# Performance work log

Measured on AMD Instinct MI355X. Metric: run time of the kernel, lower is better.

Reference implementation:

```python
import jax, jax.numpy as jnp
import numpy as np

N = 8192; E = 131072; K = 20; IN_DIM = 3; HID = 256; N_CLASSES = 32


def setup_inputs():
    key = jax.random.key(0)
    ks = jax.random.split(key, 16)

    def w(k, shape):
        lim = 1.0 / np.sqrt(shape[0])
        return jax.random.uniform(k, shape, jnp.float32, -lim, lim)

    f32 = jnp.float32
    return {
        "features": jax.random.normal(ks[0], (N, IN_DIM), f32),
        "src": jax.random.randint(ks[1], (E,), 0, N, jnp.int32),
        "dst": jax.random.randint(ks[2], (E,), 0, N, jnp.int32),
        # GraphConv params
        "Wc1": w(ks[3], (IN_DIM, HID)), "bc1": jnp.zeros((HID,), f32),
        "Wc2": w(ks[4], (HID, HID)), "bc2": jnp.zeros((HID,), f32),
        "Wc3": w(ks[5], (64, N_CLASSES)), "bc3": jnp.zeros((N_CLASSES,), f32),
        # DynamicEdgeConv 1 MLP: [2*256 -> 256 -> 256], Linear+BN+ReLU each
        "W11": w(ks[6], (2 * HID, 256)), "b11": jnp.zeros((256,), f32), "g11": jnp.ones((256,), f32), "be11": jnp.zeros((256,), f32),
        "W12": w(ks[7], (256, 256)), "b12": jnp.zeros((256,), f32), "g12": jnp.ones((256,), f32), "be12": jnp.zeros((256,), f32),
        # DynamicEdgeConv 2 MLP: [2*256 -> 64 -> 64]
        "W21": w(ks[8], (2 * 256, 64)), "b21": jnp.zeros((64,), f32), "g21": jnp.ones((64,), f32), "be21": jnp.zeros((64,), f32),
        "W22": w(ks[9], (64, 64)), "b22": jnp.zeros((64,), f32), "g22": jnp.ones((64,), f32), "be22": jnp.zeros((64,), f32),
    }


def reference(features, src, dst, Wc1, bc1, Wc2, bc2, Wc3, bc3,
              W11, b11, g11, be11, W12, b12, g12, be12,
              W21, b21, g21, be21, W22, b22, g22, be22):
    n = features.shape[0]
    ones_e = jnp.ones(src.shape[0], features.dtype)
    # DGL GraphConv norm='both': deg clamped to min 1
    dout = jnp.clip(jax.ops.segment_sum(ones_e, src, num_segments=n), 1.0) ** -0.5
    din = jnp.clip(jax.ops.segment_sum(ones_e, dst, num_segments=n), 1.0) ** -0.5

    def gconv(x, W, b, act):
        agg = jax.ops.segment_sum((x * dout[:, None])[src], dst, num_segments=n)
        r = (agg * din[:, None]) @ W + b
        return jax.nn.relu(r) if act else r

    def bn(x, g, b):  # BatchNorm1d in training mode over all edge rows
        mu = jnp.mean(x, axis=(0, 1), keepdims=True)
        var = jnp.mean(jnp.square(x - mu), axis=(0, 1), keepdims=True)
        return (x - mu) * jax.lax.rsqrt(var + 1e-5) * g + b

    def edge_conv(x, layers):
        # dynamic kNN graph on current features (self included, dist 0)
        sq = jnp.sum(x * x, axis=-1)
        d = sq[:, None] + sq[None, :] - 2.0 * (x @ x.T)  # [N,N]
        idx = jax.lax.top_k(-d, K)[1]                    # [N,K]
        xi = x[:, None, :]
        e = jnp.concatenate([jnp.broadcast_to(xi, (n, K, x.shape[-1])), x[idx] - xi], axis=-1)  # [N,K,2F]
        for W, b, g, be in layers:
            e = jax.nn.relu(bn(e @ W + b, g, be))
        return jnp.max(e, axis=1)  # max aggregation over neighbors

    h = gconv(features, Wc1, bc1, True)                                   # [N,256]
    h = edge_conv(h, [(W11, b11, g11, be11), (W12, b12, g12, be12)])      # [N,256]
    h = gconv(h, Wc2, bc2, True)                                          # [N,256]
    h = edge_conv(h, [(W21, b21, g21, be21), (W22, b22, g22, be22)])      # [N,64]
    return gconv(h, Wc3, bc3, False)                                      # [N,32]
```

## Files before the change

kernel.cpp:

```cpp
#include <hip/hip_runtime.h>

#define NN 8192
#define NE 131072
#define KNN 20
#define CH 4096
#define GBM 128
#define GBN 128
#define GBK 64

typedef __attribute__((ext_vector_type(4))) float f32x4;
typedef __attribute__((ext_vector_type(8))) __bf16 bf16x8;

__global__ void k_zero(float* p, int n){
  int i = blockIdx.x*256 + threadIdx.x;
  if (i < n) p[i] = 0.f;
}
__global__ void k_zero_i(int* p, int n){
  int i = blockIdx.x*256 + threadIdx.x;
  if (i < n) p[i] = 0;
}

__device__ __forceinline__ unsigned short f2bf(float x){
  unsigned u = __float_as_uint(x);
  unsigned r = (u + 0x7fff + ((u >> 16) & 1)) >> 16;
  return (unsigned short)r;
}
__device__ __forceinline__ float bf2f(unsigned short h){
  return __uint_as_float((unsigned)h << 16);
}
__device__ __forceinline__ void gload16(const void* g, void* l){
  __builtin_amdgcn_global_load_lds(
      (const __attribute__((address_space(1))) void*)g,
      (__attribute__((address_space(3))) void*)l, 16, 0, 0);
}

__global__ void k_count(const int* __restrict__ src, const int* __restrict__ dst,
                        int* cs, int* cd){
  int e = blockIdx.x*256 + threadIdx.x;
  if (e < NE){ atomicAdd(&cs[src[e]], 1); atomicAdd(&cd[dst[e]], 1); }
}
__global__ void k_deg(const int* cs, const int* cd, float* dout, float* din){
  int i = blockIdx.x*256 + threadIdx.x;
  if (i < NN){
    dout[i] = rsqrtf((float)max(cs[i], 1));
    din[i]  = rsqrtf((float)max(cd[i], 1));
  }
}
__global__ void k_scan(const int* __restrict__ cnt, int* __restrict__ off){
  __shared__ int sh[256];
  __shared__ int carry;
  int tid = threadIdx.x;
  if (tid == 0) carry = 0;
  __syncthreads();
  for (int base = 0; base < NN; base += 256){
    int v = cnt[base + tid];
    int x = v;
    sh[tid] = x; __syncthreads();
    for (int o = 1; o < 256; o <<= 1){
      int y = (tid >= o) ? sh[tid - o] : 0;
      __syncthreads();
      x += y; sh[tid] = x;
      __syncthreads();
    }
    off[base + tid] = carry + x - v;
    __syncthreads();
    if (tid == 255){
      carry += x;
      if (base + 256 == NN) off[NN] = carry;
    }
    __syncthreads();
  }
}
__global__ void k_fill(const int* __restrict__ src, const int* __restrict__ dst,
                       const int* __restrict__ roff, int* cursor, int* csr){
  int e = blockIdx.x*256 + threadIdx.x;
  if (e < NE){
    int d = dst[e];
    int p = atomicAdd(&cursor[d], 1);
    csr[roff[d] + p] = src[e];
  }
}

__global__ void k_gconv1(const float* __restrict__ feat, const int* __restrict__ roff,
                         const int* __restrict__ csr, const float* __restrict__ dout,
                         const float* __restrict__ din, const float* __restrict__ Wc1,
                         const float* __restrict__ bc1, float* __restrict__ h1){
  int wid = threadIdx.x >> 6, lane = threadIdx.x & 63;
  int i = blockIdx.x*4 + wid;
  float a0=0.f, a1=0.f, a2=0.f;
  int beg = roff[i], end = roff[i+1];
  for (int t = beg + lane; t < end; t += 64){
    int s = csr[t]; float w = dout[s];
    a0 += feat[s*3+0]*w; a1 += feat[s*3+1]*w; a2 += feat[s*3+2]*w;
  }
  for (int m = 32; m; m >>= 1){
    a0 += __shfl_xor(a0, m); a1 += __shfl_xor(a1, m); a2 += __shfl_xor(a2, m);
  }
  float dn = din[i];
  a0 *= dn; a1 *= dn; a2 *= dn;
  for (int c = lane; c < 256; c += 64){
    float r = a0*Wc1[c] + a1*Wc1[256+c] + a2*Wc1[512+c] + bc1[c];
    h1[(size_t)i*256 + c] = fmaxf(r, 0.f);
  }
}

__global__ void k_sq(const float* __restrict__ X, float* __restrict__ sq){
  int wid = threadIdx.x >> 6, lane = threadIdx.x & 63;
  int i = blockIdx.x*4 + wid;
  float4 v = *(const float4*)&X[(size_t)i*256 + lane*4];
  float s = v.x*v.x + v.y*v.y + v.z*v.z + v.w*v.w;
  for (int m = 32; m; m >>= 1) s += __shfl_xor(s, m);
  if (lane == 0) sq[i] = s;
}

__global__ void k_split(const float* __restrict__ X, unsigned short* __restrict__ xcat){
  int row = blockIdx.x, c = threadIdx.x;
  float x = X[(size_t)row*256 + c];
  unsigned short h = f2bf(x);
  unsigned short lo = f2bf(x - bf2f(h));
  xcat[(size_t)row*512 + c] = h;
  xcat[(size_t)row*512 + 256 + c] = lo;
}

__global__ __launch_bounds__(256)
void k_gram_mfma(const unsigned short* __restrict__ Xcat,
                 float* __restrict__ G, int r0){
  __shared__ unsigned short sA[GBM*GBK];
  __shared__ unsigned short sB[GBM*GBK];
  int tid = threadIdx.x;
  int lw = tid >> 6, l = tid & 63;
  int rbl = blockIdx.y*GBM;
  int rb = r0 + rbl;
  int cb = blockIdx.x*GBN;

  int srow = l >> 3;
  int scol = (l & 7) ^ srow;
  const unsigned short* srcA[4];
  const unsigned short* srcB[4];
  char* dstA[4]; char* dstB[4];
  #pragma unroll
  for (int i = 0; i < 4; i++){
    int c = lw*4 + i;
    int row = c*8 + srow;
    srcA[i] = Xcat + (size_t)(rb + row)*512 + scol*8;
    srcB[i] = Xcat + (size_t)(cb + row)*512 + scol*8;
    dstA[i] = (char*)sA + c*1024;
    dstB[i] = (char*)sB + c*1024;
  }

  int wm = lw >> 1, wn = lw & 1;
  int fm = l & 15, kg = l >> 4;
  unsigned offA[4][2], offB[4][2];
  #pragma unroll
  for (int mf = 0; mf < 4; mf++){
    int rowa = wm*64 + mf*16 + fm;
    int rowb = wn*64 + mf*16 + fm;
    #pragma unroll
    for (int ks = 0; ks < 2; ks++){
      offA[mf][ks] = rowa*128 + (((unsigned)(ks*4 + kg) ^ (rowa & 7)))*16;
      offB[mf][ks] = rowb*128 + (((unsigned)(ks*4 + kg) ^ (rowb & 7)))*16;
    }
  }

  f32x4 acc[4][4];
  #pragma unroll
  for (int m = 0; m < 4; m++)
    #pragma unroll
    for (int n = 0; n < 4; n++) acc[m][n] = (f32x4){0.f,0.f,0.f,0.f};

  #pragma unroll
  for (int s = 0; s < 12; s++){
    int sec = s >> 2;
    int inner = (s & 3)*64;
    int cbA = (sec == 1 ? 256 : 0) + inner;
    int cbB = (sec == 2 ? 256 : 0) + inner;
    #pragma unroll
    for (int i = 0; i < 4; i++){
      gload16(srcA[i] + cbA, dstA[i]);
      gload16(srcB[i] + cbB, dstB[i]);
    }
    __syncthreads();
    #pragma unroll
    for (int ks = 0; ks < 2; ks++){
      bf16x8 a[4], b[4];
      #pragma unroll
      for (int mf = 0; mf < 4; mf++) a[mf] = *(const bf16x8*)((const char*)sA + offA[mf][ks]);
      #pragma unroll
      for (int nf = 0; nf < 4; nf++) b[nf] = *(const bf16x8*)((const char*)sB + offB[nf][ks]);
      #pragma unroll
      for (int mf = 0; mf < 4; mf++)
        #pragma unroll
        for (int nf = 0; nf < 4; nf++)
          acc[mf][nf] = __builtin_amdgcn_mfma_f32_16x16x32_bf16(a[mf], b[nf], acc[mf][nf], 0, 0, 0);
    }
    __syncthreads();
  }

  #pragma unroll
  for (int mf = 0; mf < 4; mf++){
    int orow = rbl + wm*64 + mf*16 + kg*4;
    #pragma unroll
    for (int nf = 0; nf < 4; nf++){
      int ocol = cb + wn*64 + nf*16 + fm;
      #pragma unroll
      for (int r = 0; r < 4; r++)
        G[(size_t)(orow + r)*NN + ocol] = acc[mf][nf][r];
    }
  }
}

__global__ __launch_bounds__(256)
void k_topk(const float* __restrict__ G, const float* __restrict__ sq,
            int r0, int* __restrict__ idxo){
  __shared__ float lsq[NN];
  int tid = threadIdx.x;
  for (int t = tid; t < NN/4; t += 256)
    ((float4*)lsq)[t] = ((const float4*)sq)[t];
  __syncthreads();

  int wid = tid >> 6, lane = tid & 63;
  int rl = blockIdx.x*4 + wid;
  int gr = r0 + rl;
  const float4* row4 = (const float4*)(G + (size_t)rl*NN);
  const float4* lsq4 = (const float4*)lsq;
  float sqr = lsq[gr];

  float kd0=INFINITY,kd1=INFINITY,kd2=INFINITY,kd3=INFINITY,kd4=INFINITY,
        kd5=INFINITY,kd6=INFINITY,kd7=INFINITY,kd8=INFINITY,kd9=INFINITY,
        kd10=INFINITY,kd11=INFINITY,kd12=INFINITY,kd13=INFINITY,kd14=INFINITY,
        kd15=INFINITY,kd16=INFINITY,kd17=INFINITY,kd18=INFINITY,kd19=INFINITY;
  int ki0=0x7fffffff,ki1=0x7fffffff,ki2=0x7fffffff,ki3=0x7fffffff,ki4=0x7fffffff,
      ki5=0x7fffffff,ki6=0x7fffffff,ki7=0x7fffffff,ki8=0x7fffffff,ki9=0x7fffffff,
      ki10=0x7fffffff,ki11=0x7fffffff,ki12=0x7fffffff,ki13=0x7fffffff,ki14=0x7fffffff,
      ki15=0x7fffffff,ki16=0x7fffffff,ki17=0x7fffffff,ki18=0x7fffffff,ki19=0x7fffffff;

#define ST(U) { bool sw = nk < kd##U; float tv = kd##U; int tq = ki##U; \
      if (sw){ kd##U = nk; ki##U = ni; nk = tv; ni = tq; } }
#define INSE(kc, jc) { if ((kc) < kd19){ float nk = (kc); int ni = (jc); \
      ST(0) ST(1) ST(2) ST(3) ST(4) ST(5) ST(6) ST(7) ST(8) ST(9) \
      ST(10) ST(11) ST(12) ST(13) ST(14) ST(15) ST(16) ST(17) ST(18) ST(19) } }

  #pragma unroll 1
  for (int o = 0; o < 32; o++){
    int t4 = lane + o*64;
    float4 g = row4[t4];
    float4 s = lsq4[t4];
    int jb = t4*4;
    float k0 = (sqr + s.x) - 2.f*g.x;
    float k1 = (sqr + s.y) - 2.f*g.y;
    float k2 = (sqr + s.z) - 2.f*g.z;
    float k3 = (sqr + s.w) - 2.f*g.w;
    float t19 = kd19;
    float mn = fminf(fminf(k0,k1), fminf(k2,k3));
    if (__any(mn < t19)){
      INSE(k0, jb+0);
      INSE(k1, jb+1);
      INSE(k2, jb+2);
      INSE(k3, jb+3);
    }
  }
#undef INSE
#undef ST

#define MV(A,B) { kd##A = kd##B; ki##A = ki##B; }
  #pragma unroll 1
  for (int r = 0; r < KNN; r++){
    float bv = kd0; int bi = ki0;
    #pragma unroll
    for (int mm = 32; mm; mm >>= 1){
      float ov = __shfl_xor(bv, mm); int oi = __shfl_xor(bi, mm);
      if (ov < bv || (ov == bv && oi < bi)){ bv = ov; bi = oi; }
    }
    if (ki0 == bi){
      MV(0,1) MV(1,2) MV(2,3) MV(3,4) MV(4,5) MV(5,6) MV(6,7) MV(7,8) MV(8,9) MV(9,10)
      MV(10,11) MV(11,12) MV(12,13) MV(13,14) MV(14,15) MV(15,16) MV(16,17) MV(17,18) MV(18,19)
      kd19 = INFINITY; ki19 = 0x7fffffff;
    }
    if (lane == 0) idxo[(size_t)gr*KNN + r] = bi;
  }
#undef MV
}

__global__ void k_wd(const float* __restrict__ W, float* __restrict__ Wd, int rows, int M){
  int t = blockIdx.x*256 + threadIdx.x;
  if (t < rows*M) Wd[t] = W[t] - W[rows*M + t];
}

__global__ __launch_bounds__(256)
void k_mm(const float* __restrict__ A, const float* __restrict__ B,
          const float* __restrict__ bias, float* __restrict__ Cout,
          int n, int Kd, int M, int relu){
  __shared__ float la[16][68], lb[16][68];
  int tid = threadIdx.x;
  int rb = blockIdx.y*64, cb = blockIdx.x*64;
  int lr = tid >> 2, lq = (tid & 3)*4;
  int ty = tid >> 4, tx = tid & 15;
  float acc[4][4] = {};
  for (int k0 = 0; k0 < Kd; k0 += 16){
    __syncthreads();
    #pragma unroll
    for (int u = 0; u < 4; u++){
      int k = k0 + lq + u;
      la[lq+u][lr] = (k < Kd) ? A[(size_t)(rb+lr)*Kd + k] : 0.f;
    }
    int kk = tid >> 4; int cc = (tid & 15)*4;
    #pragma unroll
    for (int u = 0; u < 4; u++){
      int c = cb + cc + u; int k = k0 + kk;
      lb[kk][cc+u] = (k < Kd && c < M) ? B[(size_t)k*M + c] : 0.f;
    }
    __syncthreads();
    #pragma unroll
    for (int k = 0; k < 16; k++){
      float4 a = *(const float4*)&la[k][ty*4];
      float4 b = *(const float4*)&lb[k][tx*4];
      float avv[4] = {a.x,a.y,a.z,a.w}, bvv[4] = {b.x,b.y,b.z,b.w};
      #pragma unroll
      for (int u = 0; u < 4; u++)
        #pragma unroll
        for (int v = 0; v < 4; v++) acc[u][v] += avv[u]*bvv[v];
    }
  }
  #pragma unroll
  for (int u = 0; u < 4; u++){
    int r = rb + ty*4 + u;
    #pragma unroll
    for (int v = 0; v < 4; v++){
      int c = cb + tx*4 + v;
      if (c < M){
        float x = acc[u][v] + (bias ? bias[c] : 0.f);
        if (relu) x = fmaxf(x, 0.f);
        Cout[(size_t)r*M + c] = x;
      }
    }
  }
}

template<int C>
__global__ __launch_bounds__(256)
void k_stats1(const float* __restrict__ A, const float* __restrict__ P,
              const int* __restrict__ idx, float* __restrict__ ssum, float* __restrict__ ssq){
  __shared__ int si[128], sj[128];
  int tid = threadIdx.x;
  int s0 = blockIdx.x*128;
  if (tid < 128){ si[tid] = (s0 + tid)/KNN; sj[tid] = idx[s0 + tid]; }
  __syncthreads();
  constexpr int MPAR = 256/C;
  int tc = tid % C, sr = tid / C;
  float s = 0.f, q = 0.f;
  for (int m = sr; m < 128; m += MPAR){
    float v = A[(size_t)si[m]*C + tc] + P[(size_t)sj[m]*C + tc];
    s += v; q += v*v;
  }
  if constexpr (MPAR > 1){
    __shared__ float rs[256], rq[256];
    rs[tid] = s; rq[tid] = q; __syncthreads();
    if (sr == 0){
      for (int u = 1; u < MPAR; u++){ s += rs[u*C + tc]; q += rq[u*C + tc]; }
    }
  }
  if (sr == 0){ atomicAdd(&ssum[tc], s); atomicAdd(&ssq[tc], q); }
}

template<int C>
__global__ __launch_bounds__(256)
void k_colstats(const float* __restrict__ X, float* __restrict__ ssum, float* __restrict__ ssq){
  constexpr int MPAR = 256/C;
  int tid = threadIdx.x;
  int tc = tid % C, sr = tid / C;
  int base = blockIdx.x*256;
  float s = 0.f, q = 0.f;
  for (int m = sr; m < 256; m += MPAR){
    float v = X[(size_t)(base + m)*C + tc];
    s += v; q += v*v;
  }
  if constexpr (MPAR > 1){
    __shared__ float rs[256], rq[256];
    rs[tid] = s; rq[tid] = q; __syncthreads();
    if (sr == 0){
      for (int u = 1; u < MPAR; u++){ s += rs[u*C + tc]; q += rq[u*C + tc]; }
    }
  }
  if (sr == 0){ atomicAdd(&ssum[tc], s); atomicAdd(&ssq[tc], q); }
}

__global__ void k_bn_final(const float* __restrict__ ssum, const float* __restrict__ ssq,
                           const float* __restrict__ g, const float* __restrict__ be,
                           float* __restrict__ sb, float* __restrict__ tb, int C, float invn){
  int c = threadIdx.x;
  if (c < C){
    float mu = ssum[c]*invn;
    float var = fmaxf(ssq[c]*invn - mu*mu, 0.f);
    float s = g[c]*rsqrtf(var + 1e-5f);
    sb[c] = s; tb[c] = be[c] - mu*s;
  }
}

template<int C>
__global__ __launch_bounds__(256)
void k_edge_mm(const float* __restrict__ A, const float* __restrict__ P,
               const int* __restrict__ idx, const float* __restrict__ sb,
               const float* __restrict__ tb, const float* __restrict__ W,
               const float* __restrict__ bias, float* __restrict__ out){
  constexpr int BM   = (C == 256) ? 32 : 64;
  constexpr int KT   = (C == 256) ? 16 : 64;
  constexpr int COLG = C/8;
  constexpr int ROWG = 256/COLG;
  constexpr int EPT  = BM/ROWG;
  constexpr int MPAR = 256/C;
  __shared__ float e2[BM][C+1];
  __shared__ float wt[KT][C+4];
  __shared__ int sj[BM];
  int tid = threadIdx.x;
  int s0 = blockIdx.x*BM;
  if (tid < BM) sj[tid] = idx[s0 + tid];
  __syncthreads();
  for (int mb = 0; mb < BM; mb += MPAR){
    int m = mb + tid / C;
    int c = tid % C;
    int i = (s0 + m)/KNN;
    int j = sj[m];
    float v = (A[(size_t)i*C + c] + P[(size_t)j*C + c])*sb[c] + tb[c];
    e2[m][c] = fmaxf(v, 0.f);
  }
  float acc[EPT][8];
  #pragma unroll
  for (int m = 0; m < EPT; m++)
    #pragma unroll
    for (int u = 0; u < 8; u++) acc[m][u] = 0.f;
  int tr = tid / COLG, tc = tid % COLG;
  for (int kt = 0; kt < C; kt += KT){
    __syncthreads();
    for (int t = tid; t < KT*C; t += 256){
      wt[t / C][t % C] = W[(size_t)(kt + t/C)*C + (t % C)];
    }
    __syncthreads();
    #pragma unroll 4
    for (int k = 0; k < KT; k++){
      float4 w0 = *(const float4*)&wt[k][tc*8];
      float4 w1 = *(const float4*)&wt[k][tc*8 + 4];
      float b[8] = {w0.x,w0.y,w0.z,w0.w,w1.x,w1.y,w1.z,w1.w};
      #pragma unroll
      for (int m = 0; m < EPT; m++){
        float a = e2[tr*EPT + m][kt + k];
        #pragma unroll
        for (int u = 0; u < 8; u++) acc[m][u] += a*b[u];
      }
    }
  }
  #pragma unroll
  for (int m = 0; m < EPT; m++){
    int row = s0 + tr*EPT + m;
    float4 o0, o1;
    o0.x = acc[m][0] + bias[tc*8+0]; o0.y = acc[m][1] + bias[tc*8+1];
    o0.z = acc[m][2] + bias[tc*8+2]; o0.w = acc[m][3] + bias[tc*8+3];
    o1.x = acc[m][4] + bias[tc*8+4]; o1.y = acc[m][5] + bias[tc*8+5];
    o1.z = acc[m][6] + bias[tc*8+6]; o1.w = acc[m][7] + bias[tc*8+7];
    *(float4*)&out[(size_t)row*C + tc*8]     = o0;
    *(float4*)&out[(size_t)row*C + tc*8 + 4] = o1;
  }
}

template<int C>
__global__ void k_maxpool(const float* __restrict__ X, const float* __restrict__ sb,
                          const float* __restrict__ tb, float* __restrict__ H){
  constexpr int NPB = 256/C;
  int node = blockIdx.x*NPB + threadIdx.x / C;
  int c = threadIdx.x % C;
  float s = sb[c], t = tb[c];
  float mx = 0.f;
  for (int k = 0; k < KNN; k++){
    float v = X[(size_t)(node*KNN + k)*C + c]*s + t;
    mx = fmaxf(mx, v);
  }
  H[(size_t)node*C + c] = mx;
}

template<int C>
__global__ void k_agg(const float* __restrict__ X, const int* __restrict__ roff,
                      const int* __restrict__ csr, const float* __restrict__ dout,
                      const float* __restrict__ din, float* __restrict__ XA){
  int i = blockIdx.x; int c = threadIdx.x;
  float acc = 0.f;
  int b = roff[i], e = roff[i+1];
  for (int t = b; t < e; t++){
    int s = csr[t];
    acc += X[(size_t)s*C + c]*dout[s];
  }
  XA[(size_t)i*C + c] = acc*din[i];
}

extern "C" void kernel_launch(void* const* d_in, const int* in_sizes, int n_in,
                              void* d_out, int out_size, void* d_ws, size_t ws_size,
                              hipStream_t stream){
  const float* feat = (const float*)d_in[0];
  const int*   src  = (const int*)d_in[1];
  const int*   dst  = (const int*)d_in[2];
  const float* Wc1  = (const float*)d_in[3];
  const float* bc1  = (const float*)d_in[4];
  const float* Wc2  = (const float*)d_in[5];
  const float* bc2  = (const float*)d_in[6];
  const float* Wc3  = (const float*)d_in[7];
  const float* bc3  = (const float*)d_in[8];
  const float* W11  = (const float*)d_in[9];
  const float* b11  = (const float*)d_in[10];
  const float* g11  = (const float*)d_in[11];
  const float* be11 = (const float*)d_in[12];
  const float* W12  = (const float*)d_in[13];
  const float* b12  = (const float*)d_in[14];
  const float* g12  = (const float*)d_in[15];
  const float* be12 = (const float*)d_in[16];
  const float* W21  = (const float*)d_in[17];
  const float* b21  = (const float*)d_in[18];
  const float* g21  = (const float*)d_in[19];
  const float* be21 = (const float*)d_in[20];
  const float* W22  = (const float*)d_in[21];
  const float* b22  = (const float*)d_in[22];
  const float* g22  = (const float*)d_in[23];
  const float* be22 = (const float*)d_in[24];
  float* out = (float*)d_out;

  char* w = (char*)d_ws; size_t off = 0;
  auto alloc = [&](size_t bytes)->void*{
    void* p = w + off;
    off += bytes; off = (off + 255) & ~(size_t)255;
    return p;
  };
  int* cnt_s  = (int*)alloc(NN*4);
  int* cnt_d  = (int*)alloc(NN*4);
  int* roff   = (int*)alloc((NN+1)*4);
  int* cursor = (int*)alloc(NN*4);
  int* csr    = (int*)alloc(NE*4);
  int* idx    = (int*)alloc((size_t)NN*KNN*4);
  float* dout = (float*)alloc(NN*4);
  float* din  = (float*)alloc(NN*4);
  float* sqv  = (float*)alloc(NN*4);
  float* h1   = (float*)alloc((size_t)NN*256*4);
  float* h2   = (float*)alloc((size_t)NN*256*4);
  float* h3   = (float*)alloc((size_t)NN*256*4);
  float* h4   = (float*)alloc((size_t)NN*64*4);
  float* xa   = (float*)alloc((size_t)NN*256*4);
  float* Abuf = (float*)alloc((size_t)NN*256*4);
  float* Pbuf = (float*)alloc((size_t)NN*256*4);
  float* Wd   = (float*)alloc(256*256*4);
  float* ssum = (float*)alloc(256*4);
  float* ssq  = (float*)alloc(256*4);
  float* sbn  = (float*)alloc(256*4);
  float* tbn  = (float*)alloc(256*4);
  float* out2 = (float*)alloc((size_t)NN*KNN*256*4);
  float* gram = out2;
  unsigned short* xcat = (unsigned short*)(out2 + (size_t)CH*NN);
  (void)ws_size; (void)n_in; (void)in_sizes; (void)out_size;

  const float invn = 1.0f / (float)(NN*KNN);

  k_zero_i<<<32, 256, 0, stream>>>(cnt_s, NN);
  k_zero_i<<<32, 256, 0, stream>>>(cnt_d, NN);
  k_zero_i<<<32, 256, 0, stream>>>(cursor, NN);
  k_count<<<NE/256, 256, 0, stream>>>(src, dst, cnt_s, cnt_d);
  k_deg<<<32, 256, 0, stream>>>(cnt_s, cnt_d, dout, din);
  k_scan<<<1, 256, 0, stream>>>(cnt_d, roff);
  k_fill<<<NE/256, 256, 0, stream>>>(src, dst, roff, cursor, csr);

  k_gconv1<<<NN/4, 256, 0, stream>>>(feat, roff, csr, dout, din, Wc1, bc1, h1);

  k_sq<<<NN/4, 256, 0, stream>>>(h1, sqv);
  k_split<<<NN, 256, 0, stream>>>(h1, xcat);
  for (int r0 = 0; r0 < NN; r0 += CH){
    k_gram_mfma<<<dim3(NN/GBN, CH/GBM), 256, 0, stream>>>(xcat, gram, r0);
    k_topk<<<CH/4, 256, 0, stream>>>(gram, sqv, r0, idx);
  }
  k_wd<<<256, 256, 0, stream>>>(W11, Wd, 256, 256);
  k_mm<<<dim3(4, NN/64), 256, 0, stream>>>(h1, Wd, b11, Abuf, NN, 256, 256, 0);
  k_mm<<<dim3(4, NN/64), 256, 0, stream>>>(h1, W11 + 256*256, nullptr, Pbuf, NN, 256, 256, 0);
  k_zero<<<2, 256, 0, stream>>>(ssum, 256); k_zero<<<2, 256, 0, stream>>>(ssq, 256);
  k_stats1<256><<<NN*KNN/128, 256, 0, stream>>>(Abuf, Pbuf, idx, ssum, ssq);
  k_bn_final<<<1, 256, 0, stream>>>(ssum, ssq, g11, be11, sbn, tbn, 256, invn);
  k_edge_mm<256><<<NN*KNN/32, 256, 0, stream>>>(Abuf, Pbuf, idx, sbn, tbn, W12, b12, out2);
  k_zero<<<2, 256, 0, stream>>>(ssum, 256); k_zero<<<2, 256, 0, stream>>>(ssq, 256);
  k_colstats<256><<<NN*KNN/256, 256, 0, stream>>>(out2, ssum, ssq);
  k_bn_final<<<1, 256, 0, stream>>>(ssum, ssq, g12, be12, sbn, tbn, 256, invn);
  k_maxpool<256><<<NN, 256, 0, stream>>>(out2, sbn, tbn, h2);

  k_agg<256><<<NN, 256, 0, stream>>>(h2, roff, csr, dout, din, xa);
  k_mm<<<dim3(4, NN/64), 256, 0, stream>>>(xa, Wc2, bc2, h3, NN, 256, 256, 1);

  k_sq<<<NN/4, 256, 0, stream>>>(h3, sqv);
  k_split<<<NN, 256, 0, stream>>>(h3, xcat);
  for (int r0 = 0; r0 < NN; r0 += CH){
    k_gram_mfma<<<dim3(NN/GBN, CH/GBM), 256, 0, stream>>>(xcat, gram, r0);
    k_topk<<<CH/4, 256, 0, stream>>>(gram, sqv, r0, idx);
  }
  k_wd<<<64, 256, 0, stream>>>(W21, Wd, 256, 64);
  k_mm<<<dim3(1, NN/64), 256, 0, stream>>>(h3, Wd, b21, Abuf, NN, 256, 64, 0);
  k_mm<<<dim3(1, NN/64), 256, 0, stream>>>(h3, W21 + 256*64, nullptr, Pbuf, NN, 256, 64, 0);
  k_zero<<<2, 256, 0, stream>>>(ssum, 256); k_zero<<<2, 256, 0, stream>>>(ssq, 256);
  k_stats1<64><<<NN*KNN/128, 256, 0, stream>>>(Abuf, Pbuf, idx, ssum, ssq);
  k_bn_final<<<1, 256, 0, stream>>>(ssum, ssq, g21, be21, sbn, tbn, 64, invn);
  k_edge_mm<64><<<NN*KNN/64, 256, 0, stream>>>(Abuf, Pbuf, idx, sbn, tbn, W22, b22, out2);
  k_zero<<<2, 256, 0, stream>>>(ssum, 256); k_zero<<<2, 256, 0, stream>>>(ssq, 256);
  k_colstats<64><<<NN*KNN/256, 256, 0, stream>>>(out2, ssum, ssq);
  k_bn_final<<<1, 256, 0, stream>>>(ssum, ssq, g22, be22, sbn, tbn, 64, invn);
  k_maxpool<64><<<NN/4, 256, 0, stream>>>(out2, sbn, tbn, h4);

  k_agg<64><<<NN, 64, 0, stream>>>(h4, roff, csr, dout, din, xa);
  k_mm<<<dim3(1, NN/64), 256, 0, stream>>>(xa, Wc3, bc3, out, NN, 64, 32, 0);
}
```

Before: 1.604 ms.

## Use split-bf16 MFMA for first edge-conv second-layer matmul

Replaces the fp32 scalar edge matmul for the 256->256 layer with an MFMA kernel. Edge features (gather, BN, ReLU) are split into hi/lo bf16 parts in swizzled LDS. The weights are pre-split and transposed by a new kernel, and three bf16 MFMA passes (hi*hi, lo*hi, hi*lo) recover near-fp32 accuracy. This targets the FLOP-heavy 163840x256x256 GEMM, at the cost of losing the lo*lo term and doing B loads straight from global memory.

```diff
diff --git a/kernel.cpp b/kernel.cpp
--- a/kernel.cpp
+++ b/kernel.cpp
@@ -120,6 +120,15 @@
   unsigned short lo = f2bf(x - bf2f(h));
   xcat[(size_t)row*512 + c] = h;
   xcat[(size_t)row*512 + 256 + c] = lo;
+}
+
+__global__ void k_wsplit(const float* __restrict__ W, unsigned short* __restrict__ Whi,
+                         unsigned short* __restrict__ Wlo){
+  int k = blockIdx.x, n = threadIdx.x;
+  float x = W[(size_t)k*256 + n];
+  unsigned short h = f2bf(x);
+  Whi[(size_t)n*256 + k] = h;
+  Wlo[(size_t)n*256 + k] = f2bf(x - bf2f(h));
 }
 
 __global__ __launch_bounds__(256)
@@ -393,6 +402,94 @@
     float var = fmaxf(ssq[c]*invn - mu*mu, 0.f);
     float s = g[c]*rsqrtf(var + 1e-5f);
     sb[c] = s; tb[c] = be[c] - mu*s;
+  }
+}
+
+__global__ __launch_bounds__(256, 2)
+void k_edge_mfma(const float* __restrict__ A, const float* __restrict__ P,
+                 const int* __restrict__ idx, const float* __restrict__ sb,
+                 const float* __restrict__ tb, const unsigned short* __restrict__ Wthi,
+                 const unsigned short* __restrict__ Wtlo, const float* __restrict__ bias,
+                 float* __restrict__ out){
+  __shared__ unsigned short ehi[64*256];
+  __shared__ unsigned short elo[64*256];
+  __shared__ int sj[64];
+  int tid = threadIdx.x;
+  int lw = tid >> 6, l = tid & 63;
+  int s0 = blockIdx.x*64;
+  if (tid < 64) sj[tid] = idx[s0 + tid];
+  float sbc = sb[tid], tbc = tb[tid];
+  __syncthreads();
+
+  #pragma unroll 1
+  for (int it = 0; it < 64; it++){
+    int i = (s0 + it)/KNN;
+    int j = sj[it];
+    float v = (A[(size_t)i*256 + tid] + P[(size_t)j*256 + tid])*sbc + tbc;
+    v = fmaxf(v, 0.f);
+    unsigned short h = f2bf(v);
+    unsigned short lo = f2bf(v - bf2f(h));
+    unsigned off = (unsigned)it*512 + (((unsigned)tid*2) ^ (((unsigned)it & 7) << 4));
+    *(unsigned short*)((char*)ehi + off) = h;
+    *(unsigned short*)((char*)elo + off) = lo;
+  }
+  __syncthreads();
+
+  int fm = l & 15, kg = l >> 4;
+  const unsigned short* bhi[4];
+  const unsigned short* blo[4];
+  float bz[4];
+  #pragma unroll
+  for (int nf = 0; nf < 4; nf++){
+    int col = lw*64 + nf*16 + fm;
+    bhi[nf] = Wthi + (size_t)col*256 + kg*8;
+    blo[nf] = Wtlo + (size_t)col*256 + kg*8;
+    bz[nf] = bias[col];
+  }
+
+  f32x4 acc[4][4];
+  #pragma unroll
+  for (int m = 0; m < 4; m++)
+    #pragma unroll
+    for (int n = 0; n < 4; n++) acc[m][n] = (f32x4){0.f,0.f,0.f,0.f};
+
+  #pragma unroll 1
+  for (int sec = 0; sec < 3; sec++){
+    const char* abase = (sec == 1) ? (const char*)elo : (const char*)ehi;
+    int bsec = (sec == 2);
+    #pragma unroll 1
+    for (int st = 0; st < 8; st++){
+      int g = st*4 + kg;
+      bf16x8 a[4], b[4];
+      #pragma unroll
+      for (int mf = 0; mf < 4; mf++){
+        int row = mf*16 + fm;
+        a[mf] = *(const bf16x8*)(abase + row*512 + ((unsigned)(g ^ (row & 7)))*16);
+      }
+      #pragma unroll
+      for (int nf = 0; nf < 4; nf++){
+        const unsigned short* bp = bsec ? blo[nf] : bhi[nf];
+        b[nf] = *(const bf16x8*)(bp + st*32);
+      }
+      #pragma unroll
+      for (int mf = 0; mf < 4; mf++)
+        #pragma unroll
+        for (int nf = 0; nf < 4; nf++)
+          acc[mf][nf] = __builtin_amdgcn_mfma_f32_16x16x32_bf16(a[mf], b[nf], acc[mf][nf], 0, 0, 0);
+    }
+  }
+
+  #pragma unroll
+  for (int mf = 0; mf < 4; mf++){
+    #pragma unroll
+    for (int nf = 0; nf < 4; nf++){
+      int col = lw*64 + nf*16 + fm;
+      #pragma unroll
+      for (int r = 0; r < 4; r++){
+        int row = s0 + mf*16 + kg*4 + r;
+        out[(size_t)row*256 + col] = acc[mf][nf][r] + bz[nf];
+      }
+    }
   }
 }
 
@@ -547,6 +644,8 @@
   float* ssq  = (float*)alloc(256*4);
   float* sbn  = (float*)alloc(256*4);
   float* tbn  = (float*)alloc(256*4);
+  unsigned short* wthi = (unsigned short*)alloc(256*256*2);
+  unsigned short* wtlo = (unsigned short*)alloc(256*256*2);
   float* out2 = (float*)alloc((size_t)NN*KNN*256*4);
   float* gram = out2;
   unsigned short* xcat = (unsigned short*)(out2 + (size_t)CH*NN);
@@ -571,12 +670,13 @@
     k_topk<<<CH/4, 256, 0, stream>>>(gram, sqv, r0, idx);
   }
   k_wd<<<256, 256, 0, stream>>>(W11, Wd, 256, 256);
+  k_wsplit<<<256, 256, 0, stream>>>(W12, wthi, wtlo);
   k_mm<<<dim3(4, NN/64), 256, 0, stream>>>(h1, Wd, b11, Abuf, NN, 256, 256, 0);
   k_mm<<<dim3(4, NN/64), 256, 0, stream>>>(h1, W11 + 256*256, nullptr, Pbuf, NN, 256, 256, 0);
   k_zero<<<2, 256, 0, stream>>>(ssum, 256); k_zero<<<2, 256, 0, stream>>>(ssq, 256);
   k_stats1<256><<<NN*KNN/128, 256, 0, stream>>>(Abuf, Pbuf, idx, ssum, ssq);
   k_bn_final<<<1, 256, 0, stream>>>(ssum, ssq, g11, be11, sbn, tbn, 256, invn);
-  k_edge_mm<256><<<NN*KNN/32, 256, 0, stream>>>(Abuf, Pbuf, idx, sbn, tbn, W12, b12, out2);
+  k_edge_mfma<<<NN*KNN/64, 256, 0, stream>>>(Abuf, Pbuf, idx, sbn, tbn, wthi, wtlo, b12, out2);
   k_zero<<<2, 256, 0, stream>>>(ssum, 256); k_zero<<<2, 256, 0, stream>>>(ssq, 256);
   k_colstats<256><<<NN*KNN/256, 256, 0, stream>>>(out2, ssum, ssq);
   k_bn_final<<<1, 256, 0, stream>>>(ssum, ssq, g12, be12, sbn, tbn, 256, invn);
```

New measurement: 1.462 ms. 8.9% less time.
